# Kernel tuning notes

Hardware: AMD Instinct MI355X
Metric: run time of the kernel (lower is better)

Reference implementation:

```python
import jax, jax.numpy as jnp
import numpy as np

ALPHA = 2.0  # snntorch ATan surrogate default (irrelevant for fwd-only)


def _spike(x):
    return (x > 0).astype(x.dtype)


def setup_inputs() -> dict:
    key = jax.random.key(0)
    ks = jax.random.split(key, 7)
    B, T, H, O = 2048, 120, 512, 2
    sample_rate = 40.0
    x = jax.random.normal(ks[0], (B, T), dtype=jnp.float32)
    # fc1: [H, 1], fc2: [O, H] (torch Linear weight layout), gaussian init near 1/sample_rate scale
    W1 = (1.0 / sample_rate) + (0.5 / sample_rate) * jax.random.normal(ks[1], (H, 1), dtype=jnp.float32)
    W2 = (1.0 / (sample_rate * H)) + (0.5 / (sample_rate * H)) * jax.random.normal(ks[2], (O, H), dtype=jnp.float32)
    W2 = W2 * H  # keep output currents at a useful magnitude
    beta_h = 0.8 + 0.19 * jax.random.uniform(ks[3], (H,), dtype=jnp.float32)
    thr_h = 1.0 + 0.1 * jax.random.uniform(ks[4], (H,), dtype=jnp.float32)
    beta_o = 0.8 + 0.19 * jax.random.uniform(ks[5], (O,), dtype=jnp.float32)
    thr_o = 1.0 + 0.1 * jax.random.uniform(ks[6], (O,), dtype=jnp.float32)
    return {"x": x, "W1": W1, "W2": W2, "beta_h": beta_h, "thr_h": thr_h,
            "beta_o": beta_o, "thr_o": thr_o}


def reference(x, W1, W2, beta_h, thr_h, beta_o, thr_o):
    B = x.shape[0]
    H, O = W1.shape[0], W2.shape[0]
    bh = jnp.clip(beta_h, 0.0, 1.0)
    bo = jnp.clip(beta_o, 0.0, 1.0)
    w1 = W1[:, 0]  # [H]; fc1 on scalar input is an outer product

    def step(carry, x_t):
        mem1, mem2 = carry
        cur1 = x_t[:, None] * w1[None, :]              # [B, H]
        mem1 = bh * mem1 + cur1
        spk1 = _spike(mem1 - thr_h)
        mem1 = mem1 * (1.0 - spk1)                      # zero reset, no delay
        cur2 = spk1 @ W2.T                              # [B, O]
        mem2 = bo * mem2 + cur2
        spk2 = _spike(mem2 - thr_o)
        mem2 = mem2 * (1.0 - spk2)
        return (mem1, mem2), (spk1, mem1, spk2, mem2)

    init = (jnp.zeros((B, H), x.dtype), jnp.zeros((B, O), x.dtype))
    xT = x.T  # [T, B] so scan walks time steps
    _, (spk1_rec, mem1_rec, spk2_rec, mem2_rec) = jax.lax.scan(step, init, xT)
    hidden_spike_count = spk1_rec.sum()
    output_spike_count = spk2_rec.sum()
    return spk1_rec, mem1_rec, spk2_rec, mem2_rec, hidden_spike_count, output_spike_count
```

## Files before the change

kernel.cpp:

```cpp
#include <hip/hip_runtime.h>

#define T_STEPS 120
#define BATCH   2048
#define HID     512
#define OUTN    2
#define G_ROWS  8

#define SPK1_OFF 0LL
#define MEM1_OFF 125829120LL
#define SPK2_OFF 251658240LL
#define MEM2_OFF 252149760LL
#define CNT_OFF  252641280LL

typedef float f32x4 __attribute__((ext_vector_type(4)));
typedef float f32x2 __attribute__((ext_vector_type(2)));

__global__ void zero_counts_kernel(float* cnts) {
    cnts[0] = 0.0f;
    cnts[1] = 0.0f;
}

#define HSTEP(mm, bb, ww, tt, ss, ff)                                  \
    mm = __fadd_rn(__fmul_rn(bb, mm), __fmul_rn(xt, ww));              \
    const bool  ff = mm > tt;                                          \
    const float ss = ff ? 1.0f : 0.0f;                                 \
    mm = ff ? 0.0f : mm;                                               \
    hc += (int)ff;

__global__ __launch_bounds__(512) void snn_fwd_kernel(
    const float* __restrict__ x,
    const float* __restrict__ W1,
    const float* __restrict__ W2,
    const float* __restrict__ beta_h,
    const float* __restrict__ thr_h,
    const float* __restrict__ beta_o,
    const float* __restrict__ thr_o,
    float* __restrict__ spk1_rec,
    float* __restrict__ mem1_rec,
    float* __restrict__ spk2_rec,
    float* __restrict__ mem2_rec,
    float* __restrict__ cnts)
{
    const int tid  = threadIdx.x;
    const int w    = tid >> 6;
    const int lane = tid & 63;
    const int b    = blockIdx.x * G_ROWS + w;

    __shared__ float xs[G_ROWS][T_STEPS];
    __shared__ float red[G_ROWS][T_STEPS][2];

    if (lane < 60) {
        ((f32x2*)xs[w])[lane]  = ((const f32x2*)x)[(size_t)b * (T_STEPS / 2) + lane];
        ((f32x4*)red[w])[lane] = (f32x4)0.0f;
    }

    const int pA = lane;
    const int pB = 64 + lane;
    const f32x4 w1A  = ((const f32x4*)W1)[pA];
    const f32x4 w1B  = ((const f32x4*)W1)[pB];
    f32x4 bhA        = ((const f32x4*)beta_h)[pA];
    f32x4 bhB        = ((const f32x4*)beta_h)[pB];
    const f32x4 thA  = ((const f32x4*)thr_h)[pA];
    const f32x4 thB  = ((const f32x4*)thr_h)[pB];
    const f32x4 w20A = ((const f32x4*)W2)[pA];
    const f32x4 w20B = ((const f32x4*)W2)[pB];
    const f32x4 w21A = ((const f32x4*)(W2 + HID))[pA];
    const f32x4 w21B = ((const f32x4*)(W2 + HID))[pB];
    bhA.x = fminf(fmaxf(bhA.x, 0.0f), 1.0f);
    bhA.y = fminf(fmaxf(bhA.y, 0.0f), 1.0f);
    bhA.z = fminf(fmaxf(bhA.z, 0.0f), 1.0f);
    bhA.w = fminf(fmaxf(bhA.w, 0.0f), 1.0f);
    bhB.x = fminf(fmaxf(bhB.x, 0.0f), 1.0f);
    bhB.y = fminf(fmaxf(bhB.y, 0.0f), 1.0f);
    bhB.z = fminf(fmaxf(bhB.z, 0.0f), 1.0f);
    bhB.w = fminf(fmaxf(bhB.w, 0.0f), 1.0f);

    float mA0 = 0.f, mA1 = 0.f, mA2 = 0.f, mA3 = 0.f;
    float mB0 = 0.f, mB1 = 0.f, mB2 = 0.f, mB3 = 0.f;
    int hc = 0;

    __syncthreads();

    const size_t st1 = (size_t)BATCH * HID;
    float* sp = spk1_rec + (size_t)b * HID + (size_t)lane * 4;
    float* mp = mem1_rec + (size_t)b * HID + (size_t)lane * 4;

    #pragma unroll 2
    for (int t = 0; t < T_STEPS; ++t) {
        const float xt = xs[w][t];

        HSTEP(mA0, bhA.x, w1A.x, thA.x, sA0, fA0)
        HSTEP(mA1, bhA.y, w1A.y, thA.y, sA1, fA1)
        HSTEP(mA2, bhA.z, w1A.z, thA.z, sA2, fA2)
        HSTEP(mA3, bhA.w, w1A.w, thA.w, sA3, fA3)
        HSTEP(mB0, bhB.x, w1B.x, thB.x, sB0, fB0)
        HSTEP(mB1, bhB.y, w1B.y, thB.y, sB1, fB1)
        HSTEP(mB2, bhB.z, w1B.z, thB.z, sB2, fB2)
        HSTEP(mB3, bhB.w, w1B.w, thB.w, sB3, fB3)

        f32x4 sAv; sAv.x = sA0; sAv.y = sA1; sAv.z = sA2; sAv.w = sA3;
        f32x4 sBv; sBv.x = sB0; sBv.y = sB1; sBv.z = sB2; sBv.w = sB3;
        f32x4 mAv; mAv.x = mA0; mAv.y = mA1; mAv.z = mA2; mAv.w = mA3;
        f32x4 mBv; mBv.x = mB0; mBv.y = mB1; mBv.z = mB2; mBv.w = mB3;
        __builtin_nontemporal_store(sAv, (f32x4*)sp);
        __builtin_nontemporal_store(sBv, (f32x4*)(sp + 256));
        __builtin_nontemporal_store(mAv, (f32x4*)mp);
        __builtin_nontemporal_store(mBv, (f32x4*)(mp + 256));
        sp += st1;
        mp += st1;

        if (__ballot(fA0 | fA1 | fA2 | fA3 | fB0 | fB1 | fB2 | fB3) != 0ULL) {
            float c0 = sA0 * w20A.x + sA1 * w20A.y + sA2 * w20A.z + sA3 * w20A.w
                     + sB0 * w20B.x + sB1 * w20B.y + sB2 * w20B.z + sB3 * w20B.w;
            float c1 = sA0 * w21A.x + sA1 * w21A.y + sA2 * w21A.z + sA3 * w21A.w
                     + sB0 * w21B.x + sB1 * w21B.y + sB2 * w21B.z + sB3 * w21B.w;
            #pragma unroll
            for (int o = 32; o > 0; o >>= 1) {
                c0 += __shfl_down(c0, o, 64);
                c1 += __shfl_down(c1, o, 64);
            }
            if (lane == 0) { red[w][t][0] = c0; red[w][t][1] = c1; }
        }
    }

    float fc = (float)hc;
    #pragma unroll
    for (int o = 32; o > 0; o >>= 1) fc += __shfl_down(fc, o, 64);
    if (lane == 0) atomicAdd(&cnts[0], fc);

    if (lane < OUTN) {
        const int o = lane;
        const float bo = fminf(fmaxf(beta_o[o], 0.0f), 1.0f);
        const float to = thr_o[o];
        float m = 0.0f;
        int oc = 0;
        const size_t st2 = (size_t)BATCH * OUTN;
        float* s2p = spk2_rec + (size_t)b * OUTN + o;
        float* m2p = mem2_rec + (size_t)b * OUTN + o;
        #pragma unroll 4
        for (int t = 0; t < T_STEPS; ++t) {
            const float cur = red[w][t][o];
            m = __fadd_rn(__fmul_rn(bo, m), cur);
            const bool f = m > to;
            s2p[0] = f ? 1.0f : 0.0f;
            if (f) { m = 0.0f; oc++; }
            m2p[0] = m;
            s2p += st2;
            m2p += st2;
        }
        if (oc) atomicAdd(&cnts[1], (float)oc);
    }
}

extern "C" void kernel_launch(void* const* d_in, const int* in_sizes, int n_in,
                              void* d_out, int out_size, void* d_ws, size_t ws_size,
                              hipStream_t stream) {
    const float* x      = (const float*)d_in[0];
    const float* W1     = (const float*)d_in[1];
    const float* W2     = (const float*)d_in[2];
    const float* beta_h = (const float*)d_in[3];
    const float* thr_h  = (const float*)d_in[4];
    const float* beta_o = (const float*)d_in[5];
    const float* thr_o  = (const float*)d_in[6];

    float* out  = (float*)d_out;
    float* spk1 = out + SPK1_OFF;
    float* mem1 = out + MEM1_OFF;
    float* spk2 = out + SPK2_OFF;
    float* mem2 = out + MEM2_OFF;
    float* cnts = out + CNT_OFF;

    zero_counts_kernel<<<1, 1, 0, stream>>>(cnts);

    snn_fwd_kernel<<<BATCH / G_ROWS, 512, 0, stream>>>(
        x, W1, W2, beta_h, thr_h, beta_o, thr_o,
        spk1, mem1, spk2, mem2, cnts);
}
```

Before: 1.008 ms.

## Stage output-layer records in shared memory and replace atomics with two-pass count reduction

The output-neuron recurrence now writes its spike and membrane records into shared-memory tiles, which the whole block then stores cooperatively. Before, two lanes per wave issued strided scalar stores. The global atomics and the zeroing kernel are replaced by per-block partial counts in workspace plus a small deterministic reduction kernel. This adds a block-wide barrier and a second launch. The bulk of the traffic is the hidden-layer records, so the effect on total time is likely minor.

```diff
diff --git a/kernel.cpp b/kernel.cpp
--- a/kernel.cpp
+++ b/kernel.cpp
@@ -5,6 +5,7 @@
 #define HID     512
 #define OUTN    2
 #define G_ROWS  8
+#define NBLK    (BATCH / G_ROWS)
 
 #define SPK1_OFF 0LL
 #define MEM1_OFF 125829120LL
@@ -15,9 +16,26 @@
 typedef float f32x4 __attribute__((ext_vector_type(4)));
 typedef float f32x2 __attribute__((ext_vector_type(2)));
 
-__global__ void zero_counts_kernel(float* cnts) {
-    cnts[0] = 0.0f;
-    cnts[1] = 0.0f;
+__global__ __launch_bounds__(256) void count_reduce_kernel(
+    const float* __restrict__ ws, float* __restrict__ cnts)
+{
+    const int tid  = threadIdx.x;
+    const int w    = tid >> 6;
+    const int lane = tid & 63;
+    float h = ws[tid];
+    float o = ws[NBLK + tid];
+    #pragma unroll
+    for (int off = 32; off > 0; off >>= 1) {
+        h += __shfl_down(h, off, 64);
+        o += __shfl_down(o, off, 64);
+    }
+    __shared__ float sh[4][2];
+    if (lane == 0) { sh[w][0] = h; sh[w][1] = o; }
+    __syncthreads();
+    if (tid == 0) {
+        cnts[0] = sh[0][0] + sh[1][0] + sh[2][0] + sh[3][0];
+        cnts[1] = sh[0][1] + sh[1][1] + sh[2][1] + sh[3][1];
+    }
 }
 
 #define HSTEP(mm, bb, ww, tt, ss, ff)                                  \
@@ -39,7 +57,7 @@
     float* __restrict__ mem1_rec,
     float* __restrict__ spk2_rec,
     float* __restrict__ mem2_rec,
-    float* __restrict__ cnts)
+    float* __restrict__ ws)
 {
     const int tid  = threadIdx.x;
     const int w    = tid >> 6;
@@ -48,6 +66,10 @@
 
     __shared__ float xs[G_ROWS][T_STEPS];
     __shared__ float red[G_ROWS][T_STEPS][2];
+    __shared__ float s2tile[T_STEPS][G_ROWS * OUTN];
+    __shared__ float m2tile[T_STEPS][G_ROWS * OUTN];
+    __shared__ float redc[G_ROWS];
+    __shared__ float redo[G_ROWS];
 
     if (lane < 60) {
         ((f32x2*)xs[w])[lane]  = ((const f32x2*)x)[(size_t)b * (T_STEPS / 2) + lane];
@@ -126,29 +148,47 @@
     float fc = (float)hc;
     #pragma unroll
     for (int o = 32; o > 0; o >>= 1) fc += __shfl_down(fc, o, 64);
-    if (lane == 0) atomicAdd(&cnts[0], fc);
-
+    if (lane == 0) redc[w] = fc;
+
+    float ocf = 0.0f;
     if (lane < OUTN) {
         const int o = lane;
         const float bo = fminf(fmaxf(beta_o[o], 0.0f), 1.0f);
         const float to = thr_o[o];
         float m = 0.0f;
-        int oc = 0;
-        const size_t st2 = (size_t)BATCH * OUTN;
-        float* s2p = spk2_rec + (size_t)b * OUTN + o;
-        float* m2p = mem2_rec + (size_t)b * OUTN + o;
         #pragma unroll 4
         for (int t = 0; t < T_STEPS; ++t) {
             const float cur = red[w][t][o];
             m = __fadd_rn(__fmul_rn(bo, m), cur);
             const bool f = m > to;
-            s2p[0] = f ? 1.0f : 0.0f;
-            if (f) { m = 0.0f; oc++; }
-            m2p[0] = m;
-            s2p += st2;
-            m2p += st2;
+            if (f) { m = 0.0f; ocf += 1.0f; }
+            s2tile[t][w * OUTN + o] = f ? 1.0f : 0.0f;
+            m2tile[t][w * OUTN + o] = m;
         }
-        if (oc) atomicAdd(&cnts[1], (float)oc);
+    }
+    ocf += __shfl_down(ocf, 1, 64);
+    if (lane == 0) redo[w] = ocf;
+
+    __syncthreads();
+
+    if (tid == 0) {
+        float th_ = 0.f, to_ = 0.f;
+        #pragma unroll
+        for (int i = 0; i < G_ROWS; ++i) { th_ += redc[i]; to_ += redo[i]; }
+        ws[blockIdx.x]        = th_;
+        ws[NBLK + blockIdx.x] = to_;
+    }
+
+    const size_t base2 = (size_t)blockIdx.x * G_ROWS * OUTN;
+    const float* s2t = &s2tile[0][0];
+    const float* m2t = &m2tile[0][0];
+    #pragma unroll
+    for (int e = tid; e < T_STEPS * G_ROWS * OUTN; e += 512) {
+        const int t = e >> 4;
+        const int c = e & 15;
+        const size_t g = (size_t)t * (BATCH * OUTN) + base2 + c;
+        spk2_rec[g] = s2t[e];
+        mem2_rec[g] = m2t[e];
     }
 }
 
@@ -169,10 +209,11 @@
     float* spk2 = out + SPK2_OFF;
     float* mem2 = out + MEM2_OFF;
     float* cnts = out + CNT_OFF;
-
-    zero_counts_kernel<<<1, 1, 0, stream>>>(cnts);
-
-    snn_fwd_kernel<<<BATCH / G_ROWS, 512, 0, stream>>>(
+    float* wsf  = (float*)d_ws;
+
+    snn_fwd_kernel<<<NBLK, 512, 0, stream>>>(
         x, W1, W2, beta_h, thr_h, beta_o, thr_o,
-        spk1, mem1, spk2, mem2, cnts);
+        spk1, mem1, spk2, mem2, wsf);
+
+    count_reduce_kernel<<<1, 256, 0, stream>>>(wsf, cnts);
 }
```

After: 1.002 ms. About the same (-0.6%).
